# Performance work log

Measured on AMD Instinct MI355X. Metric: run time of the kernel, lower is better.

The kernel has to match this reference:

```python
import jax, jax.numpy as jnp
import numpy as np

B = 512      # batch of scenes
K = 16       # entities (slots) per scene
H = 500      # h == HIDDEN_SIZE (required by fc2 input width 2*HIDDEN_SIZE)
A = 64       # action_size
EPS = 1e-5


def layernorm(x, g, b):
    mu = jnp.mean(x, axis=-1, keepdims=True)
    var = jnp.var(x, axis=-1, keepdims=True)
    return (x - mu) * jax.lax.rsqrt(var + EPS) * g + b


def setup_inputs() -> dict:
    key = jax.random.key(0)
    ks = jax.random.split(key, 40)
    def W(i, shape, scale=0.02):
        return (jax.random.normal(ks[i], shape, dtype=jnp.float32) * scale)
    inp = {
        "state": jax.random.normal(ks[0], (B * K, H), dtype=jnp.float32),
        "actions": jax.random.normal(ks[1], (B, A), dtype=jnp.float32),
        # action path
        "ac_fc1_w": W(2, (A, H)), "ac_fc1_b": jnp.zeros((H,), jnp.float32),
        "ac_ln1_g": jnp.ones((H,), jnp.float32), "ac_ln1_b": jnp.zeros((H,), jnp.float32),
        "ac_fc2_w": W(3, (2 * H, H)), "ac_fc2_b": jnp.zeros((H,), jnp.float32),
        "ac_lnf2_w": W(4, (H, H)), "ac_lnf2_b": jnp.zeros((H,), jnp.float32),  # ac_ln_f2 is a Linear in the source
        "ac_fc3_w": W(5, (2 * H, 1)), "ac_fc3_b": jnp.zeros((1,), jnp.float32),
        # main path
        "fc1_w": W(6, (H, H)), "fc1_b": jnp.zeros((H,), jnp.float32),
        "ln1_g": jnp.ones((H,), jnp.float32), "ln1_b": jnp.zeros((H,), jnp.float32),
        "fc2_w": W(7, (2 * H, H)), "fc2_b": jnp.zeros((H,), jnp.float32),
        "ln2_g": jnp.ones((H,), jnp.float32), "ln2_b": jnp.zeros((H,), jnp.float32),
        "fc3_w": W(8, (H, H)), "fc3_b": jnp.zeros((H,), jnp.float32),
        "ln3_g": jnp.ones((H,), jnp.float32), "ln3_b": jnp.zeros((H,), jnp.float32),
        "fc4_w": W(9, (H, 100)), "fc4_b": jnp.zeros((100,), jnp.float32),
        "ln4_g": jnp.ones((100,), jnp.float32), "ln4_b": jnp.zeros((100,), jnp.float32),
        "fc5_w": W(10, (100, 1)), "fc5_b": jnp.zeros((1,), jnp.float32),
        "fc6_w": W(11, (2 * H, H)), "fc6_b": jnp.zeros((H,), jnp.float32),
        "ln6_g": jnp.ones((H,), jnp.float32), "ln6_b": jnp.zeros((H,), jnp.float32),
    }
    return inp


def reference(state, actions,
              ac_fc1_w, ac_fc1_b, ac_ln1_g, ac_ln1_b,
              ac_fc2_w, ac_fc2_b, ac_lnf2_w, ac_lnf2_b, ac_fc3_w, ac_fc3_b,
              fc1_w, fc1_b, ln1_g, ln1_b,
              fc2_w, fc2_b, ln2_g, ln2_b,
              fc3_w, fc3_b, ln3_g, ln3_b,
              fc4_w, fc4_b, ln4_g, ln4_b,
              fc5_w, fc5_b,
              fc6_w, fc6_b, ln6_g, ln6_b):
    b, k, h, nc = B, K, H, K - 1

    # ---- action_forward (has_action=True) ----
    a = layernorm(actions @ ac_fc1_w + ac_fc1_b, ac_ln1_g, ac_ln1_b)      # [b, h]
    a = jnp.broadcast_to(a[:, None, :], (b, k, h)).reshape(b * k, h)       # repeat over k
    concat_a = jnp.concatenate([state, a], axis=1)                          # [b*k, 2h]
    attention_a = jax.nn.sigmoid(concat_a @ ac_fc3_w + ac_fc3_b)           # [b*k, 1]
    effect = (concat_a @ ac_fc2_w + ac_fc2_b) @ ac_lnf2_w + ac_lnf2_b      # ac_ln_f2 is Linear
    state = effect * attention_a                                            # [b*k, h]

    # ---- per-entity encoder ----
    s1 = jax.nn.relu(layernorm(state @ fc1_w + fc1_b, ln1_g, ln1_b))       # [b*k, h]
    s1r = s1.reshape(b, k, h)

    # ---- all-pairs context gather: for each i, all j != i ----
    idx = np.array([[j for j in range(k) if j != i] for i in range(k)])    # [k, k-1] static
    cs = s1r[:, idx, :]                                                     # [b, k, k-1, h]
    fs = jnp.broadcast_to(s1r[:, :, None, :], (b, k, nc, h))               # [b, k, k-1, h]
    pair = jnp.concatenate([fs, cs], axis=-1).reshape(b * k * nc, 2 * h)   # [b*k*(k-1), 2h]

    # ---- edge MLP ----
    core = jax.nn.relu(layernorm(pair @ fc2_w + fc2_b, ln2_g, ln2_b))      # [b*k*nc, h]
    context = jax.nn.relu(layernorm(core @ fc3_w + fc3_b, ln3_g, ln3_b))
    context = context.reshape(b * k, nc, h)

    # ---- attention-weighted sum aggregation ----
    att = jnp.tanh(layernorm(core @ fc4_w + fc4_b, ln4_g, ln4_b))          # [b*k*nc, 100]
    att = jax.nn.sigmoid(att @ fc5_w + fc5_b).reshape(b * k, nc, 1)
    effect_sum = jnp.sum(context * att, axis=1)                             # [b*k, h]

    # ---- update ----
    total = jnp.concatenate([s1, effect_sum], axis=1)                       # [b*k, 2h]
    h_new = layernorm(total @ fc6_w + fc6_b, ln6_g, ln6_b)                  # [b*k, h]
    return h_new
```

## Files before the change

### kernel.cpp

```cpp
#include <hip/hip_runtime.h>
#include <math.h>


#define EPSF 1e-5f
typedef unsigned short u16;
typedef unsigned int u32;

typedef __bf16 bf16x8 __attribute__((ext_vector_type(8)));
typedef float f32x4 __attribute__((ext_vector_type(4)));
typedef u16 u16x8 __attribute__((ext_vector_type(8)));

__device__ __forceinline__ float bf2f(u16 u) {
  return __builtin_bit_cast(float, (u32)u << 16);
}
__device__ __forceinline__ u16 f2bf(float f) {
  u32 u = __builtin_bit_cast(u32, f);
  return (u16)((u + 0x7FFFu + ((u >> 16) & 1u)) >> 16);
}

#define GLOAD16(g, l) __builtin_amdgcn_global_load_lds( \
    (__attribute__((address_space(1))) u32*)(g), \
    (__attribute__((address_space(3))) u32*)(l), 16, 0, 0)

template <typename TOUT>
__global__ __launch_bounds__(256) void gemm_mfma(
    const u16* __restrict__ A, const u16* __restrict__ Bt,
    const float* __restrict__ bias, const float* __restrict__ rowscale,
    TOUT* __restrict__ C, int M, int Npad, int K)
{
  __shared__ __align__(16) u16 As[2][128 * 64];
  __shared__ __align__(16) u16 Bs[2][64 * 64];
  const int tid = threadIdx.x;
  const int lane = tid & 63, wid = tid >> 6;

  const int ncols = gridDim.x;
  const int nwg = ncols * gridDim.y;
  const int bid = blockIdx.y * ncols + blockIdx.x;
  const int swz = (bid & 7) * (nwg >> 3) + (bid >> 3);
  const size_t row0 = (size_t)(swz / ncols) * 128;
  const size_t col0 = (size_t)(swz % ncols) * 64;

  f32x4 acc[2][4] = {};

  const int s_sub = tid >> 3;
  const int s_chunk = (tid & 7) ^ (s_sub & 7);
  const u16* gA = A + (row0 + s_sub) * (size_t)K + s_chunk * 8;
  const u16* gB = Bt + (col0 + s_sub) * (size_t)K + s_chunk * 8;

  const int fr = lane & 15, fq = lane >> 4;
  const int cx0 = fq ^ (fr & 7);
  const int cx1 = (4 + fq) ^ (fr & 7);

  const int nkt = K >> 6;
  int cur = 0;

  {
    const u16* a = gA; const u16* b = gB;
#pragma unroll
    for (int h = 0; h < 4; ++h)
      GLOAD16(a + (size_t)h * 32 * K, &As[0][(h * 256 + tid) * 8]);
#pragma unroll
    for (int h = 0; h < 2; ++h)
      GLOAD16(b + (size_t)h * 32 * K, &Bs[0][(h * 256 + tid) * 8]);
  }
  __syncthreads();

  for (int kt = 0; kt < nkt; ++kt) {
    if (kt + 1 < nkt) {
      const u16* a = gA + (size_t)(kt + 1) * 64;
      const u16* b = gB + (size_t)(kt + 1) * 64;
#pragma unroll
      for (int h = 0; h < 4; ++h)
        GLOAD16(a + (size_t)h * 32 * K, &As[cur ^ 1][(h * 256 + tid) * 8]);
#pragma unroll
      for (int h = 0; h < 2; ++h)
        GLOAD16(b + (size_t)h * 32 * K, &Bs[cur ^ 1][(h * 256 + tid) * 8]);
    }
    const u16* as = As[cur];
    const u16* bs = Bs[cur];
#pragma unroll
    for (int ks = 0; ks < 2; ++ks) {
      const int cx = ks ? cx1 : cx0;
      bf16x8 af[2], bf[4];
#pragma unroll
      for (int m = 0; m < 2; ++m) {
        int row = wid * 32 + m * 16 + fr;
        af[m] = *reinterpret_cast<const bf16x8*>(as + (row * 8 + cx) * 8);
      }
#pragma unroll
      for (int n = 0; n < 4; ++n) {
        int row = n * 16 + fr;
        bf[n] = *reinterpret_cast<const bf16x8*>(bs + (row * 8 + cx) * 8);
      }
#pragma unroll
      for (int m = 0; m < 2; ++m)
#pragma unroll
        for (int n = 0; n < 4; ++n)
          acc[m][n] = __builtin_amdgcn_mfma_f32_16x16x32_bf16(af[m], bf[n], acc[m][n], 0, 0, 0);
    }
    __syncthreads();
    cur ^= 1;
  }

  const int cl = lane & 15, rg = lane >> 4;
#pragma unroll
  for (int m = 0; m < 2; ++m) {
#pragma unroll
    for (int n = 0; n < 4; ++n) {
      size_t col = col0 + n * 16 + cl;
      float bv = bias[col];
#pragma unroll
      for (int r = 0; r < 4; ++r) {
        size_t row = row0 + wid * 32 + m * 16 + rg * 4 + r;
        float v = acc[m][n][r] + bv;
        if (rowscale) v *= rowscale[row];
        if constexpr (sizeof(TOUT) == 2) C[row * Npad + col] = f2bf(v);
        else                             C[row * Npad + col] = v;
      }
    }
  }
}

__global__ __launch_bounds__(256) void gemm128(
    const float* __restrict__ A, const float* __restrict__ B,
    const float* __restrict__ bias, float* __restrict__ C, int M, int N, int K)
{
  __shared__ float As[16][132];
  __shared__ float Bs[16][128];
  const int tid = threadIdx.x;
  const int tx = tid & 15, ty = tid >> 4;
  const int row0 = blockIdx.y * 128, col0 = blockIdx.x * 128;
  float acc[8][8];
#pragma unroll
  for (int i = 0; i < 8; ++i)
#pragma unroll
    for (int j = 0; j < 8; ++j) acc[i][j] = 0.f;

  const int nkt = (K + 15) >> 4;
  for (int kt = 0; kt < nkt; ++kt) {
    const int k0 = kt << 4;
#pragma unroll
    for (int h = 0; h < 2; ++h) {
      int i = tid + h * 256;
      int m = i >> 2, kk = (i & 3) << 2;
      int gm = row0 + m, gk = k0 + kk;
      float4 v = make_float4(0.f, 0.f, 0.f, 0.f);
      if (gm < M && gk < K) v = *reinterpret_cast<const float4*>(A + (size_t)gm * K + gk);
      As[kk + 0][m] = v.x; As[kk + 1][m] = v.y; As[kk + 2][m] = v.z; As[kk + 3][m] = v.w;
    }
#pragma unroll
    for (int h = 0; h < 2; ++h) {
      int i = tid + h * 256;
      int kk = i >> 5, n = (i & 31) << 2;
      int gk = k0 + kk, gn = col0 + n;
      float4 v = make_float4(0.f, 0.f, 0.f, 0.f);
      if (gk < K && gn < N) v = *reinterpret_cast<const float4*>(B + (size_t)gk * N + gn);
      *reinterpret_cast<float4*>(&Bs[kk][n]) = v;
    }
    __syncthreads();
#pragma unroll
    for (int kk = 0; kk < 16; ++kk) {
      float4 a0 = *reinterpret_cast<const float4*>(&As[kk][ty * 4]);
      float4 a1 = *reinterpret_cast<const float4*>(&As[kk][ty * 4 + 64]);
      float4 b0 = *reinterpret_cast<const float4*>(&Bs[kk][tx * 4]);
      float4 b1 = *reinterpret_cast<const float4*>(&Bs[kk][tx * 4 + 64]);
      float av[8] = {a0.x, a0.y, a0.z, a0.w, a1.x, a1.y, a1.z, a1.w};
      float bv[8] = {b0.x, b0.y, b0.z, b0.w, b1.x, b1.y, b1.z, b1.w};
#pragma unroll
      for (int i = 0; i < 8; ++i)
#pragma unroll
        for (int j = 0; j < 8; ++j) acc[i][j] += av[i] * bv[j];
    }
    __syncthreads();
  }
#pragma unroll
  for (int i = 0; i < 8; ++i) {
    int gm = row0 + ty * 4 + ((i >> 2) << 6) + (i & 3);
    if (gm >= M) continue;
#pragma unroll
    for (int j = 0; j < 8; ++j) {
      int gn = col0 + tx * 4 + ((j >> 2) << 6) + (j & 3);
      if (gn < N) C[(size_t)gm * N + gn] = acc[i][j] + bias[gn];
    }
  }
}

template <int ACT, typename TOUT>
__global__ __launch_bounds__(256) void ln_wave4(
    const float* __restrict__ X, TOUT* __restrict__ Y,
    const float* __restrict__ g, const float* __restrict__ b,
    int ldx, int ldy)
{
  int w = threadIdx.x >> 6, lane = threadIdx.x & 63;
  int id0 = (blockIdx.x * 4 + w) * 4;
  int k0 = lane * 8;
  float xv[4][8], s[4], s2[4];
#pragma unroll
  for (int r = 0; r < 4; ++r) {
    const float* x = X + (size_t)(id0 + r) * ldx;
    if (k0 + 8 <= 500) {
      float4 a = *reinterpret_cast<const float4*>(x + k0);
      float4 c = *reinterpret_cast<const float4*>(x + k0 + 4);
      xv[r][0] = a.x; xv[r][1] = a.y; xv[r][2] = a.z; xv[r][3] = a.w;
      xv[r][4] = c.x; xv[r][5] = c.y; xv[r][6] = c.z; xv[r][7] = c.w;
    } else {
#pragma unroll
      for (int e = 0; e < 8; ++e) xv[r][e] = (k0 + e < 500) ? x[k0 + e] : 0.f;
    }
    s[r] = 0.f; s2[r] = 0.f;
#pragma unroll
    for (int e = 0; e < 8; ++e) { s[r] += xv[r][e]; s2[r] += xv[r][e] * xv[r][e]; }
  }
#pragma unroll
  for (int m = 32; m; m >>= 1)
#pragma unroll
    for (int r = 0; r < 4; ++r) {
      s[r] += __shfl_xor(s[r], m);
      s2[r] += __shfl_xor(s2[r], m);
    }
  float gv[8], bv[8];
#pragma unroll
  for (int e = 0; e < 8; ++e) {
    int k = k0 + e;
    gv[e] = (k < 500) ? g[k] : 0.f;
    bv[e] = (k < 500) ? b[k] : 0.f;
  }
#pragma unroll
  for (int r = 0; r < 4; ++r) {
    float mu = s[r] / 500.f;
    float rstd = rsqrtf(s2[r] / 500.f - mu * mu + EPSF);
    float ov[8];
#pragma unroll
    for (int e = 0; e < 8; ++e) {
      float v = (k0 + e < 500) ? ((xv[r][e] - mu) * rstd * gv[e] + bv[e]) : 0.f;
      if (ACT == 1) v = fmaxf(v, 0.f);
      ov[e] = v;
    }
    if constexpr (sizeof(TOUT) == 2) {
      u16x8 o;
#pragma unroll
      for (int e = 0; e < 8; ++e) o[e] = f2bf(ov[e]);
      *reinterpret_cast<u16x8*>((u16*)Y + (size_t)(id0 + r) * ldy + k0) = o;
    } else {
      float* y = (float*)Y + (size_t)(id0 + r) * ldy;
      if (k0 + 4 <= 500)
        *reinterpret_cast<float4*>(y + k0) = make_float4(ov[0], ov[1], ov[2], ov[3]);
      if (k0 + 8 <= 500)
        *reinterpret_cast<float4*>(y + k0 + 4) = make_float4(ov[4], ov[5], ov[6], ov[7]);
    }
  }
}

__global__ __launch_bounds__(256) void build_concat(
    const float* __restrict__ state, const u16* __restrict__ a, u16* __restrict__ cat)
{
  int r = blockIdx.x, t = threadIdx.x;
  int b = r >> 4;
  u16* c = cat + (size_t)r * 1024;
  if (t < 125) {
    float4 v = *reinterpret_cast<const float4*>(state + (size_t)r * 500 + t * 4);
    ushort4 o; o.x = f2bf(v.x); o.y = f2bf(v.y); o.z = f2bf(v.z); o.w = f2bf(v.w);
    *reinterpret_cast<ushort4*>(c + t * 4) = o;
    *reinterpret_cast<ushort4*>(c + 500 + t * 4) =
        *reinterpret_cast<const ushort4*>(a + (size_t)b * 512 + t * 4);
  }
  if (t < 24) c[1000 + t] = 0;
}

__global__ __launch_bounds__(256) void build_total(
    const u16* __restrict__ s1, const float* __restrict__ esum, u16* __restrict__ tot)
{
  int r = blockIdx.x, t = threadIdx.x;
  u16* c = tot + (size_t)r * 1024;
  if (t < 125) {
    *reinterpret_cast<ushort4*>(c + t * 4) =
        *reinterpret_cast<const ushort4*>(s1 + (size_t)r * 512 + t * 4);
    float4 v = *reinterpret_cast<const float4*>(esum + (size_t)r * 500 + t * 4);
    ushort4 o; o.x = f2bf(v.x); o.y = f2bf(v.y); o.z = f2bf(v.z); o.w = f2bf(v.w);
    *reinterpret_cast<ushort4*>(c + 512 + t * 4) = o;
  }
  if (t < 12) { c[500 + t] = 0; c[1012 + t] = 0; }
}

__global__ __launch_bounds__(256) void dot_sig4(
    const u16* __restrict__ cat, const float* __restrict__ w3,
    const float* __restrict__ b3, float* __restrict__ atta)
{
  int w = threadIdx.x >> 6, lane = threadIdx.x & 63;
  int r0 = (blockIdx.x * 4 + w) * 4;
  int k0 = lane * 16;
  float wv[16];
#pragma unroll
  for (int e = 0; e < 16; ++e) wv[e] = (k0 + e < 1000) ? w3[k0 + e] : 0.f;
  float s[4];
#pragma unroll
  for (int r = 0; r < 4; ++r) {
    const u16* x = cat + (size_t)(r0 + r) * 1024 + k0;
    u16x8 u0 = *reinterpret_cast<const u16x8*>(x);
    u16x8 u1 = *reinterpret_cast<const u16x8*>(x + 8);
    float acc = 0.f;
#pragma unroll
    for (int e = 0; e < 8; ++e) acc += bf2f(u0[e]) * wv[e];
#pragma unroll
    for (int e = 0; e < 8; ++e) acc += bf2f(u1[e]) * wv[8 + e];
    s[r] = acc;
  }
#pragma unroll
  for (int m = 32; m; m >>= 1)
#pragma unroll
    for (int r = 0; r < 4; ++r) s[r] += __shfl_xor(s[r], m);
  if (lane == 0) {
#pragma unroll
    for (int r = 0; r < 4; ++r)
      atta[r0 + r] = 1.f / (1.f + expf(-(s[r] + b3[0])));
  }
}

__global__ __launch_bounds__(256) void core_build3(
    const u16* __restrict__ PQ, u16* __restrict__ core,
    const float* __restrict__ g2, const float* __restrict__ b2, int c0)
{
  int w = threadIdx.x >> 6, lane = threadIdx.x & 63;
  int id0 = (blockIdx.x * 4 + w) * 4;
  int k0 = lane * 8;
  u16x8 up[4], uq[4];
#pragma unroll
  for (int r = 0; r < 4; ++r) {
    int id = id0 + r;
    int pp = id / 15, j = id - pp * 15;
    int gp = c0 + pp, i = gp & 15;
    int col = j + (j >= i);
    int r2 = (gp & ~15) | col;
    up[r] = *reinterpret_cast<const u16x8*>(PQ + (size_t)gp * 1024 + k0);
    uq[r] = *reinterpret_cast<const u16x8*>(PQ + (size_t)r2 * 1024 + 512 + k0);
  }
  float xv[4][8], s[4], s2[4];
#pragma unroll
  for (int r = 0; r < 4; ++r) {
    s[r] = 0.f; s2[r] = 0.f;
#pragma unroll
    for (int e = 0; e < 8; ++e) {
      float v = bf2f(up[r][e]) + bf2f(uq[r][e]);
      xv[r][e] = v; s[r] += v; s2[r] += v * v;
    }
  }
#pragma unroll
  for (int m = 32; m; m >>= 1)
#pragma unroll
    for (int r = 0; r < 4; ++r) {
      s[r] += __shfl_xor(s[r], m);
      s2[r] += __shfl_xor(s2[r], m);
    }
  float gv[8], bv[8];
#pragma unroll
  for (int e = 0; e < 8; ++e) {
    int k = k0 + e;
    gv[e] = (k < 500) ? g2[k] : 0.f;
    bv[e] = (k < 500) ? b2[k] : 0.f;
  }
#pragma unroll
  for (int r = 0; r < 4; ++r) {
    float mu = s[r] / 500.f;
    float rstd = rsqrtf(s2[r] / 500.f - mu * mu + EPSF);
    u16x8 o;
#pragma unroll
    for (int e = 0; e < 8; ++e)
      o[e] = (k0 + e < 500) ? f2bf(fmaxf((xv[r][e] - mu) * rstd * gv[e] + bv[e], 0.f)) : (u16)0;
    *reinterpret_cast<u16x8*>(core + (size_t)(id0 + r) * 512 + k0) = o;
  }
}

__global__ __launch_bounds__(256) void chunk_post3(
    const u16* __restrict__ V,
    const float* __restrict__ g3, const float* __restrict__ b3,
    const float* __restrict__ g4, const float* __restrict__ b4,
    const float* __restrict__ w5, const float* __restrict__ b5,
    float* __restrict__ esum, int c0)
{
  __shared__ u16 rows[15][512];
  __shared__ float st[15][4];
  int pp = blockIdx.x, t = threadIdx.x;
  int lane = t & 63, w = t >> 6;
  int k0 = lane * 8;
  int kk = lane * 2;

  u16x8 u[4]; ushort2 ua[4];
#pragma unroll
  for (int r = 0; r < 4; ++r) {
    int j = w * 4 + r;
    if (j < 15) {
      const u16* vr = V + (size_t)(pp * 15 + j) * 640;
      u[r] = *reinterpret_cast<const u16x8*>(vr + k0);
      ua[r] = *reinterpret_cast<const ushort2*>(vr + 512 + kk);
    }
  }
  float s[4], s2[4], sa[4], sa2[4], y0[4], y1[4];
#pragma unroll
  for (int r = 0; r < 4; ++r) {
    s[r] = s2[r] = sa[r] = sa2[r] = 0.f; y0[r] = y1[r] = 0.f;
    int j = w * 4 + r;
    if (j < 15) {
#pragma unroll
      for (int e = 0; e < 8; ++e) { float v = bf2f(u[r][e]); s[r] += v; s2[r] += v * v; }
      y0[r] = bf2f(ua[r].x); y1[r] = bf2f(ua[r].y);
      sa[r] = y0[r] + y1[r]; sa2[r] = y0[r] * y0[r] + y1[r] * y1[r];
      *reinterpret_cast<u16x8*>(&rows[j][k0]) = u[r];
    }
  }
#pragma unroll
  for (int m = 32; m; m >>= 1)
#pragma unroll
    for (int r = 0; r < 4; ++r) {
      s[r]   += __shfl_xor(s[r], m);
      s2[r]  += __shfl_xor(s2[r], m);
      sa[r]  += __shfl_xor(sa[r], m);
      sa2[r] += __shfl_xor(sa2[r], m);
    }
  float dv[4];
#pragma unroll
  for (int r = 0; r < 4; ++r) {
    float mu4 = sa[r] / 100.f;
    float rstd4 = rsqrtf(sa2[r] / 100.f - mu4 * mu4 + EPSF);
    float d = 0.f;
    if (kk < 100)     d += tanhf((y0[r] - mu4) * rstd4 * g4[kk] + b4[kk]) * w5[kk];
    if (kk + 1 < 100) d += tanhf((y1[r] - mu4) * rstd4 * g4[kk + 1] + b4[kk + 1]) * w5[kk + 1];
    dv[r] = d;
  }
#pragma unroll
  for (int m = 32; m; m >>= 1)
#pragma unroll
    for (int r = 0; r < 4; ++r) dv[r] += __shfl_xor(dv[r], m);
  if (lane == 0) {
#pragma unroll
    for (int r = 0; r < 4; ++r) {
      int j = w * 4 + r;
      if (j < 15) {
        float mu = s[r] / 500.f;
        st[j][0] = mu;
        st[j][1] = rsqrtf(s2[r] / 500.f - mu * mu + EPSF);
        st[j][2] = 1.f / (1.f + expf(-(dv[r] + b5[0])));
      }
    }
  }
  __syncthreads();

  for (int n = t; n < 500; n += 256) {
    float gg = g3[n], bb = b3[n], acc = 0.f;
#pragma unroll
    for (int j = 0; j < 15; ++j) {
      float v = bf2f(rows[j][n]);
      acc += fmaxf((v - st[j][0]) * st[j][1] * gg + bb, 0.f) * st[j][2];
    }
    esum[(size_t)(c0 + pp) * 500 + n] = acc;
  }
}

struct TJob {
  const float* src; u16* dst;
  int K, N, srcLd, ldDst, nOff, kOff, tileBase, tilesX;
};
struct TJobs { TJob j[9]; int total; };

__global__ void pack_weights(TJobs jobs)
{
  __shared__ float tl[32][33];
  int bid = blockIdx.x;
  int ji = 0;
#pragma unroll
  for (int q = 1; q < 9; ++q) if (bid >= jobs.j[q].tileBase) ji = q;
  const TJob& J = jobs.j[ji];
  int t = bid - J.tileBase;
  int bx = t % J.tilesX, by = t / J.tilesX;
  int tx = threadIdx.x, ty = threadIdx.y;
  int k0 = by * 32, n0 = bx * 32;
#pragma unroll
  for (int r = 0; r < 4; ++r) {
    int row = k0 + ty + r * 8;
    if (row < J.K && n0 + tx < J.N) tl[ty + r * 8][tx] = J.src[(size_t)row * J.srcLd + n0 + tx];
  }
  __syncthreads();
#pragma unroll
  for (int r = 0; r < 4; ++r) {
    int n = n0 + ty + r * 8, k = k0 + tx;
    if (n < J.N && k < J.K)
      J.dst[(size_t)(n + J.nOff) * J.ldDst + J.kOff + k] = f2bf(tl[tx][ty + r * 8]);
  }
}

__global__ void pack_biases(
    const float* ac2, const float* lnf2, const float* f1, const float* f2,
    const float* f3, const float* f4, const float* f6,
    float* b_ac2p, float* b_lnf2p, float* b_f1p, float* b2p, float* b34p, float* b_f6p)
{
  int t = threadIdx.x;
  switch (blockIdx.x) {
    case 0: if (t < 512) b_ac2p[t]  = (t < 500) ? ac2[t]  : 0.f; break;
    case 1: if (t < 512) b_lnf2p[t] = (t < 500) ? lnf2[t] : 0.f; break;
    case 2: if (t < 512) b_f1p[t]   = (t < 500) ? f1[t]   : 0.f; break;
    case 3: b2p[t] = (t < 500) ? f2[t] : 0.f; break;
    case 4: if (t < 640) b34p[t] = (t < 500) ? f3[t] : ((t >= 512 && t < 612) ? f4[t - 512] : 0.f); break;
    case 5: if (t < 512) b_f6p[t]   = (t < 500) ? f6[t]   : 0.f; break;
  }
}

extern "C" void kernel_launch(void* const* d_in, const int* in_sizes, int n_in,
                              void* d_out, int out_size, void* d_ws, size_t ws_size,
                              hipStream_t stream)
{
  const float* state    = (const float*)d_in[0];
  const float* actions  = (const float*)d_in[1];
  const float* ac_fc1_w = (const float*)d_in[2];
  const float* ac_fc1_b = (const float*)d_in[3];
  const float* ac_ln1_g = (const float*)d_in[4];
  const float* ac_ln1_b = (const float*)d_in[5];
  const float* ac_fc2_w = (const float*)d_in[6];
  const float* ac_fc2_b = (const float*)d_in[7];
  const float* ac_lnf2_w= (const float*)d_in[8];
  const float* ac_lnf2_b= (const float*)d_in[9];
  const float* ac_fc3_w = (const float*)d_in[10];
  const float* ac_fc3_b = (const float*)d_in[11];
  const float* fc1_w = (const float*)d_in[12];
  const float* fc1_b = (const float*)d_in[13];
  const float* ln1_g = (const float*)d_in[14];
  const float* ln1_b = (const float*)d_in[15];
  const float* fc2_w = (const float*)d_in[16];
  const float* fc2_b = (const float*)d_in[17];
  const float* ln2_g = (const float*)d_in[18];
  const float* ln2_b = (const float*)d_in[19];
  const float* fc3_w = (const float*)d_in[20];
  const float* fc3_b = (const float*)d_in[21];
  const float* ln3_g = (const float*)d_in[22];
  const float* ln3_b = (const float*)d_in[23];
  const float* fc4_w = (const float*)d_in[24];
  const float* fc4_b = (const float*)d_in[25];
  const float* ln4_g = (const float*)d_in[26];
  const float* ln4_b = (const float*)d_in[27];
  const float* fc5_w = (const float*)d_in[28];
  const float* fc5_b = (const float*)d_in[29];
  const float* fc6_w = (const float*)d_in[30];
  const float* fc6_b = (const float*)d_in[31];
  const float* ln6_g = (const float*)d_in[32];
  const float* ln6_b = (const float*)d_in[33];
  float* out = (float*)d_out;

  char* p = (char*)d_ws;
  auto carve = [&](size_t bytes) { char* r = p; p += (bytes + 255) & ~(size_t)255; return r; };
  u16*   cat    = (u16*)  carve(8192ull * 1024 * 2);
  u16*   t1     = (u16*)  carve(8192ull * 512 * 2);
  u16*   s2     = (u16*)  carve(8192ull * 512 * 2);
  u16*   s1     = (u16*)  carve(8192ull * 512 * 2);
  u16*   core   = (u16*)  carve(30720ull * 512 * 2);
  u16*   v      = (u16*)  carve(30720ull * 640 * 2);
  float* pre    = (float*)carve(8192ull * 512 * 4);
  u16*   PQ     = (u16*)  carve(8192ull * 1024 * 2);
  float* esum   = (float*)carve(8192ull * 500 * 4);
  u16*   a_buf  = (u16*)  carve(512ull * 512 * 2);
  float* tmp_a  = (float*)carve(512ull * 500 * 4);
  float* att_a  = (float*)carve(8192ull * 4);
  char*  wT0    =         carve(0);
  u16*   ac_fc2T  = (u16*)carve(512ull * 1024 * 2);
  u16*   ac_lnf2T = (u16*)carve(512ull * 512 * 2);
  u16*   fc1T     = (u16*)carve(512ull * 512 * 2);
  u16*   B2T      = (u16*)carve(1024ull * 512 * 2);
  u16*   B34T     = (u16*)carve(640ull * 512 * 2);
  u16*   fc6T     = (u16*)carve(512ull * 1024 * 2);
  size_t wTbytes  = (size_t)((char*)carve(0) - wT0);
  float* b_ac2p  = (float*)carve(512 * 4);
  float* b_lnf2p = (float*)carve(512 * 4);
  float* b_f1p   = (float*)carve(512 * 4);
  float* b2p     = (float*)carve(1024 * 4);
  float* b34p    = (float*)carve(640 * 4);
  float* b_f6p   = (float*)carve(512 * 4);

  dim3 blk(256);
  dim3 tblk(32, 8);

  hipMemsetAsync(wT0, 0, wTbytes, stream);
  TJobs jobs;
  int base = 0;
  auto addjob = [&](int idx, const float* src, u16* dst, int K, int N, int srcLd,
                    int ldDst, int nOff, int kOff) {
    int tx = (N + 31) / 32, ty = (K + 31) / 32;
    jobs.j[idx] = {src, dst, K, N, srcLd, ldDst, nOff, kOff, base, tx};
    base += tx * ty;
  };
  addjob(0, ac_fc2_w,         ac_fc2T,  1000, 500, 500, 1024, 0, 0);
  addjob(1, ac_lnf2_w,        ac_lnf2T,  500, 500, 500,  512, 0, 0);
  addjob(2, fc1_w,            fc1T,      500, 500, 500,  512, 0, 0);
  addjob(3, fc2_w,            B2T,       500, 500, 500,  512, 0, 0);
  addjob(4, fc2_w + 250000,   B2T,       500, 500, 500,  512, 512, 0);
  addjob(5, fc3_w,            B34T,      500, 500, 500,  512, 0, 0);
  addjob(6, fc4_w,            B34T,      500, 100, 100,  512, 512, 0);
  addjob(7, fc6_w,            fc6T,      500, 500, 500, 1024, 0, 0);
  addjob(8, fc6_w + 250000,   fc6T,      500, 500, 500, 1024, 0, 512);
  jobs.total = base;
  pack_weights<<<base, tblk, 0, stream>>>(jobs);
  pack_biases<<<6, 1024, 0, stream>>>(ac_fc2_b, ac_lnf2_b, fc1_b, fc2_b, fc3_b, fc4_b, fc6_b,
                                      b_ac2p, b_lnf2p, b_f1p, b2p, b34p, b_f6p);

  gemm128<<<dim3(4, 4), blk, 0, stream>>>(actions, ac_fc1_w, ac_fc1_b, tmp_a, 512, 500, 64);
  ln_wave4<0, u16><<<32, blk, 0, stream>>>(tmp_a, a_buf, ac_ln1_g, ac_ln1_b, 500, 512);
  build_concat<<<8192, blk, 0, stream>>>(state, a_buf, cat);

  gemm_mfma<u16><<<dim3(8, 64), blk, 0, stream>>>(cat, ac_fc2T, b_ac2p, nullptr, t1, 8192, 512, 1024);
  dot_sig4<<<512, blk, 0, stream>>>(cat, ac_fc3_w, ac_fc3_b, att_a);
  gemm_mfma<u16><<<dim3(8, 64), blk, 0, stream>>>(t1, ac_lnf2T, b_lnf2p, att_a, s2, 8192, 512, 512);
  gemm_mfma<float><<<dim3(8, 64), blk, 0, stream>>>(s2, fc1T, b_f1p, nullptr, pre, 8192, 512, 512);
  ln_wave4<1, u16><<<512, blk, 0, stream>>>(pre, s1, ln1_g, ln1_b, 512, 512);
  gemm_mfma<u16><<<dim3(16, 64), blk, 0, stream>>>(s1, B2T, b2p, nullptr, PQ, 8192, 1024, 512);

  for (int c = 0; c < 4; ++c) {
    int c0 = c * 2048;
    core_build3<<<1920, blk, 0, stream>>>(PQ, core, ln2_g, ln2_b, c0);
    gemm_mfma<u16><<<dim3(10, 240), blk, 0, stream>>>(core, B34T, b34p, nullptr, v, 30720, 640, 512);
    chunk_post3<<<2048, blk, 0, stream>>>(v, ln3_g, ln3_b, ln4_g, ln4_b, fc5_w, fc5_b, esum, c0);
  }

  build_total<<<8192, blk, 0, stream>>>(s1, esum, cat);
  gemm_mfma<float><<<dim3(8, 64), blk, 0, stream>>>(cat, fc6T, b_f6p, nullptr, pre, 8192, 512, 1024);
  ln_wave4<0, float><<<512, blk, 0, stream>>>(pre, out, ln6_g, ln6_b, 512, 500);
}
```

Before: 490.4 us.

## Split-source A in GEMM, bf16 intermediates, fewer chunks, finer waitcnt sync

The MFMA GEMM can now read its A operand from two separate buffers split at a K offset, so the final fc6 GEMM reads s1 and esum directly and the build_total concat kernel is dropped. GEMM outputs and the LayerNorm inputs move from fp32 to bf16, and esum is written as bf16. This cuts memory traffic but adds bf16 rounding before the LayerNorms. The edge-MLP loop runs 2 chunks of 4096 instead of 4 of 2048, which means fewer launches and larger buffers. The pipeline syncs switch to explicit vmcnt/lgkmcnt waits with raw barriers, letting the next tile's loads stay in flight across the barrier.

Result: faster. 428.2 us (-12.7%).

```diff
diff --git a/kernel.cpp b/kernel.cpp
--- a/kernel.cpp
+++ b/kernel.cpp
@@ -24,9 +24,10 @@
 
 template <typename TOUT>
 __global__ __launch_bounds__(256) void gemm_mfma(
-    const u16* __restrict__ A, const u16* __restrict__ Bt,
+    const u16* __restrict__ A, const u16* __restrict__ A2,
+    const u16* __restrict__ Bt,
     const float* __restrict__ bias, const float* __restrict__ rowscale,
-    TOUT* __restrict__ C, int M, int Npad, int K)
+    TOUT* __restrict__ C, int M, int Npad, int K, int lda, int khalf)
 {
   __shared__ __align__(16) u16 As[2][128 * 64];
   __shared__ __align__(16) u16 Bs[2][64 * 64];
@@ -44,7 +45,9 @@
 
   const int s_sub = tid >> 3;
   const int s_chunk = (tid & 7) ^ (s_sub & 7);
-  const u16* gA = A + (row0 + s_sub) * (size_t)K + s_chunk * 8;
+  const size_t aoff = (row0 + s_sub) * (size_t)lda + s_chunk * 8;
+  const u16* gA = A + aoff;
+  const u16* gA2 = A2 ? (A2 + aoff - khalf) : nullptr;
   const u16* gB = Bt + (col0 + s_sub) * (size_t)K + s_chunk * 8;
 
   const int fr = lane & 15, fq = lane >> 4;
@@ -55,27 +58,33 @@
   int cur = 0;
 
   {
-    const u16* a = gA; const u16* b = gB;
 #pragma unroll
     for (int h = 0; h < 4; ++h)
-      GLOAD16(a + (size_t)h * 32 * K, &As[0][(h * 256 + tid) * 8]);
+      GLOAD16(gA + (size_t)h * 32 * lda, &As[0][(h * 256 + tid) * 8]);
 #pragma unroll
     for (int h = 0; h < 2; ++h)
-      GLOAD16(b + (size_t)h * 32 * K, &Bs[0][(h * 256 + tid) * 8]);
-  }
-  __syncthreads();
+      GLOAD16(gB + (size_t)h * 32 * K, &Bs[0][(h * 256 + tid) * 8]);
+  }
 
   for (int kt = 0; kt < nkt; ++kt) {
     if (kt + 1 < nkt) {
-      const u16* a = gA + (size_t)(kt + 1) * 64;
-      const u16* b = gB + (size_t)(kt + 1) * 64;
+      const int kk = (kt + 1) * 64;
+      const u16* a = (A2 && kk >= khalf) ? (gA2 + kk) : (gA + kk);
+      const u16* b = gB + kk;
 #pragma unroll
       for (int h = 0; h < 4; ++h)
-        GLOAD16(a + (size_t)h * 32 * K, &As[cur ^ 1][(h * 256 + tid) * 8]);
+        GLOAD16(a + (size_t)h * 32 * lda, &As[cur ^ 1][(h * 256 + tid) * 8]);
 #pragma unroll
       for (int h = 0; h < 2; ++h)
         GLOAD16(b + (size_t)h * 32 * K, &Bs[cur ^ 1][(h * 256 + tid) * 8]);
-    }
+      asm volatile("s_waitcnt vmcnt(6)" ::: "memory");
+    } else {
+      asm volatile("s_waitcnt vmcnt(0)" ::: "memory");
+    }
+    __builtin_amdgcn_sched_barrier(0);
+    __builtin_amdgcn_s_barrier();
+    __builtin_amdgcn_sched_barrier(0);
+
     const u16* as = As[cur];
     const u16* bs = Bs[cur];
 #pragma unroll
@@ -98,7 +107,10 @@
         for (int n = 0; n < 4; ++n)
           acc[m][n] = __builtin_amdgcn_mfma_f32_16x16x32_bf16(af[m], bf[n], acc[m][n], 0, 0, 0);
     }
-    __syncthreads();
+    asm volatile("s_waitcnt lgkmcnt(0)" ::: "memory");
+    __builtin_amdgcn_sched_barrier(0);
+    __builtin_amdgcn_s_barrier();
+    __builtin_amdgcn_sched_barrier(0);
     cur ^= 1;
   }
 
@@ -185,9 +197,9 @@
   }
 }
 
-template <int ACT, typename TOUT>
+template <int ACT, typename TIN, typename TOUT>
 __global__ __launch_bounds__(256) void ln_wave4(
-    const float* __restrict__ X, TOUT* __restrict__ Y,
+    const TIN* __restrict__ X, TOUT* __restrict__ Y,
     const float* __restrict__ g, const float* __restrict__ b,
     int ldx, int ldy)
 {
@@ -197,17 +209,23 @@
   float xv[4][8], s[4], s2[4];
 #pragma unroll
   for (int r = 0; r < 4; ++r) {
-    const float* x = X + (size_t)(id0 + r) * ldx;
-    if (k0 + 8 <= 500) {
-      float4 a = *reinterpret_cast<const float4*>(x + k0);
-      float4 c = *reinterpret_cast<const float4*>(x + k0 + 4);
-      xv[r][0] = a.x; xv[r][1] = a.y; xv[r][2] = a.z; xv[r][3] = a.w;
-      xv[r][4] = c.x; xv[r][5] = c.y; xv[r][6] = c.z; xv[r][7] = c.w;
+    s[r] = 0.f; s2[r] = 0.f;
+    if constexpr (sizeof(TIN) == 2) {
+      u16x8 u = *reinterpret_cast<const u16x8*>((const u16*)X + (size_t)(id0 + r) * ldx + k0);
+#pragma unroll
+      for (int e = 0; e < 8; ++e) xv[r][e] = bf2f(u[e]);
     } else {
-#pragma unroll
-      for (int e = 0; e < 8; ++e) xv[r][e] = (k0 + e < 500) ? x[k0 + e] : 0.f;
-    }
-    s[r] = 0.f; s2[r] = 0.f;
+      const float* x = (const float*)X + (size_t)(id0 + r) * ldx;
+      if (k0 + 8 <= 500) {
+        float4 a = *reinterpret_cast<const float4*>(x + k0);
+        float4 c = *reinterpret_cast<const float4*>(x + k0 + 4);
+        xv[r][0] = a.x; xv[r][1] = a.y; xv[r][2] = a.z; xv[r][3] = a.w;
+        xv[r][4] = c.x; xv[r][5] = c.y; xv[r][6] = c.z; xv[r][7] = c.w;
+      } else {
+#pragma unroll
+        for (int e = 0; e < 8; ++e) xv[r][e] = (k0 + e < 500) ? x[k0 + e] : 0.f;
+      }
+    }
 #pragma unroll
     for (int e = 0; e < 8; ++e) { s[r] += xv[r][e]; s2[r] += xv[r][e] * xv[r][e]; }
   }
@@ -267,21 +285,6 @@
   if (t < 24) c[1000 + t] = 0;
 }
 
-__global__ __launch_bounds__(256) void build_total(
-    const u16* __restrict__ s1, const float* __restrict__ esum, u16* __restrict__ tot)
-{
-  int r = blockIdx.x, t = threadIdx.x;
-  u16* c = tot + (size_t)r * 1024;
-  if (t < 125) {
-    *reinterpret_cast<ushort4*>(c + t * 4) =
-        *reinterpret_cast<const ushort4*>(s1 + (size_t)r * 512 + t * 4);
-    float4 v = *reinterpret_cast<const float4*>(esum + (size_t)r * 500 + t * 4);
-    ushort4 o; o.x = f2bf(v.x); o.y = f2bf(v.y); o.z = f2bf(v.z); o.w = f2bf(v.w);
-    *reinterpret_cast<ushort4*>(c + 512 + t * 4) = o;
-  }
-  if (t < 12) { c[500 + t] = 0; c[1012 + t] = 0; }
-}
-
 __global__ __launch_bounds__(256) void dot_sig4(
     const u16* __restrict__ cat, const float* __restrict__ w3,
     const float* __restrict__ b3, float* __restrict__ atta)
@@ -375,7 +378,7 @@
     const float* __restrict__ g3, const float* __restrict__ b3,
     const float* __restrict__ g4, const float* __restrict__ b4,
     const float* __restrict__ w5, const float* __restrict__ b5,
-    float* __restrict__ esum, int c0)
+    u16* __restrict__ esum16, int c0)
 {
   __shared__ u16 rows[15][512];
   __shared__ float st[15][4];
@@ -444,6 +447,7 @@
   }
   __syncthreads();
 
+  u16* o = esum16 + (size_t)(c0 + pp) * 512;
   for (int n = t; n < 500; n += 256) {
     float gg = g3[n], bb = b3[n], acc = 0.f;
 #pragma unroll
@@ -451,8 +455,9 @@
       float v = bf2f(rows[j][n]);
       acc += fmaxf((v - st[j][0]) * st[j][1] * gg + bb, 0.f) * st[j][2];
     }
-    esum[(size_t)(c0 + pp) * 500 + n] = acc;
-  }
+    o[n] = f2bf(acc);
+  }
+  if (t < 12) o[500 + t] = 0;
 }
 
 struct TJob {
@@ -549,11 +554,10 @@
   u16*   t1     = (u16*)  carve(8192ull * 512 * 2);
   u16*   s2     = (u16*)  carve(8192ull * 512 * 2);
   u16*   s1     = (u16*)  carve(8192ull * 512 * 2);
-  u16*   core   = (u16*)  carve(30720ull * 512 * 2);
-  u16*   v      = (u16*)  carve(30720ull * 640 * 2);
-  float* pre    = (float*)carve(8192ull * 512 * 4);
+  u16*   core   = (u16*)  carve(61440ull * 512 * 2);
+  u16*   v      = (u16*)  carve(61440ull * 640 * 2);
   u16*   PQ     = (u16*)  carve(8192ull * 1024 * 2);
-  float* esum   = (float*)carve(8192ull * 500 * 4);
+  u16*   esum16 = (u16*)  carve(8192ull * 512 * 2);
   u16*   a_buf  = (u16*)  carve(512ull * 512 * 2);
   float* tmp_a  = (float*)carve(512ull * 500 * 4);
   float* att_a  = (float*)carve(8192ull * 4);
@@ -599,24 +603,30 @@
                                       b_ac2p, b_lnf2p, b_f1p, b2p, b34p, b_f6p);
 
   gemm128<<<dim3(4, 4), blk, 0, stream>>>(actions, ac_fc1_w, ac_fc1_b, tmp_a, 512, 500, 64);
-  ln_wave4<0, u16><<<32, blk, 0, stream>>>(tmp_a, a_buf, ac_ln1_g, ac_ln1_b, 500, 512);
+  ln_wave4<0, float, u16><<<32, blk, 0, stream>>>(tmp_a, a_buf, ac_ln1_g, ac_ln1_b, 500, 512);
   build_concat<<<8192, blk, 0, stream>>>(state, a_buf, cat);
 
-  gemm_mfma<u16><<<dim3(8, 64), blk, 0, stream>>>(cat, ac_fc2T, b_ac2p, nullptr, t1, 8192, 512, 1024);
+  gemm_mfma<u16><<<dim3(8, 64), blk, 0, stream>>>(cat, nullptr, ac_fc2T, b_ac2p, nullptr,
+                                                  t1, 8192, 512, 1024, 1024, 0);
   dot_sig4<<<512, blk, 0, stream>>>(cat, ac_fc3_w, ac_fc3_b, att_a);
-  gemm_mfma<u16><<<dim3(8, 64), blk, 0, stream>>>(t1, ac_lnf2T, b_lnf2p, att_a, s2, 8192, 512, 512);
-  gemm_mfma<float><<<dim3(8, 64), blk, 0, stream>>>(s2, fc1T, b_f1p, nullptr, pre, 8192, 512, 512);
-  ln_wave4<1, u16><<<512, blk, 0, stream>>>(pre, s1, ln1_g, ln1_b, 512, 512);
-  gemm_mfma<u16><<<dim3(16, 64), blk, 0, stream>>>(s1, B2T, b2p, nullptr, PQ, 8192, 1024, 512);
-
-  for (int c = 0; c < 4; ++c) {
-    int c0 = c * 2048;
-    core_build3<<<1920, blk, 0, stream>>>(PQ, core, ln2_g, ln2_b, c0);
-    gemm_mfma<u16><<<dim3(10, 240), blk, 0, stream>>>(core, B34T, b34p, nullptr, v, 30720, 640, 512);
-    chunk_post3<<<2048, blk, 0, stream>>>(v, ln3_g, ln3_b, ln4_g, ln4_b, fc5_w, fc5_b, esum, c0);
-  }
-
-  build_total<<<8192, blk, 0, stream>>>(s1, esum, cat);
-  gemm_mfma<float><<<dim3(8, 64), blk, 0, stream>>>(cat, fc6T, b_f6p, nullptr, pre, 8192, 512, 1024);
-  ln_wave4<0, float><<<512, blk, 0, stream>>>(pre, out, ln6_g, ln6_b, 512, 500);
-}
+  gemm_mfma<u16><<<dim3(8, 64), blk, 0, stream>>>(t1, nullptr, ac_lnf2T, b_lnf2p, att_a,
+                                                  s2, 8192, 512, 512, 512, 0);
+  gemm_mfma<u16><<<dim3(8, 64), blk, 0, stream>>>(s2, nullptr, fc1T, b_f1p, nullptr,
+                                                  t1, 8192, 512, 512, 512, 0);
+  ln_wave4<1, u16, u16><<<512, blk, 0, stream>>>(t1, s1, ln1_g, ln1_b, 512, 512);
+  gemm_mfma<u16><<<dim3(16, 64), blk, 0, stream>>>(s1, nullptr, B2T, b2p, nullptr,
+                                                   PQ, 8192, 1024, 512, 512, 0);
+
+  for (int c = 0; c < 2; ++c) {
+    int c0 = c * 4096;
+    core_build3<<<3840, blk, 0, stream>>>(PQ, core, ln2_g, ln2_b, c0);
+    gemm_mfma<u16><<<dim3(10, 480), blk, 0, stream>>>(core, nullptr, B34T, b34p, nullptr,
+                                                      v, 61440, 640, 512, 512, 0);
+    chunk_post3<<<4096, blk, 0, stream>>>(v, ln3_g, ln3_b, ln4_g, ln4_b, fc5_w, fc5_b,
+                                          esum16, c0);
+  }
+
+  gemm_mfma<u16><<<dim3(8, 64), blk, 0, stream>>>(s1, esum16, fc6T, b_f6p, nullptr,
+                                                  t1, 8192, 512, 1024, 512, 512);
+  ln_wave4<0, u16, float><<<512, blk, 0, stream>>>(t1, out, ln6_g, ln6_b, 512, 500);
+}
```
